# Optimization experiments

Hardware: AMD Instinct MI355X
Metric: run time of the kernel (lower is better)

Reference implementation:

```python
import jax, jax.numpy as jnp
import numpy as np

D_MODEL = 1024
N_HEADS = 16
D_K = D_MODEL // N_HEADS


def setup_inputs() -> dict:
    key = jax.random.key(0)
    ks = jax.random.split(key, 5)
    B, T = 4, 2048
    scale = 1.0 / np.sqrt(D_MODEL)
    return {
        "x": jax.random.normal(ks[0], (B, T, D_MODEL), dtype=jnp.float32),
        "W_q": jax.random.normal(ks[1], (D_MODEL, D_MODEL), dtype=jnp.float32) * scale,
        "W_k": jax.random.normal(ks[2], (D_MODEL, D_MODEL), dtype=jnp.float32) * scale,
        "W_v": jax.random.normal(ks[3], (D_MODEL, D_MODEL), dtype=jnp.float32) * scale,
        "W_o": jax.random.normal(ks[4], (D_MODEL, D_MODEL), dtype=jnp.float32) * scale,
    }


def reference(x, W_q, W_k, W_v, W_o):
    B, T, C = x.shape
    # torch nn.Linear(bias=False): y = x @ W.T
    def proj(W):
        y = jnp.einsum('btc,dc->btd', x, W)
        # (B, T, H, Dk) -> (B, H, T, Dk)
        return y.reshape(B, T, N_HEADS, D_K).transpose(0, 2, 1, 3)

    Q, K, V = proj(W_q), proj(W_k), proj(W_v)
    scores = jnp.einsum('bhqd,bhkd->bhqk', Q, K) / jnp.sqrt(jnp.float32(D_K))
    # causal mask: disallow k > q
    causal = jnp.triu(jnp.ones((T, T), dtype=bool), k=1)
    scores = jnp.where(causal, -jnp.inf, scores)
    attn = jax.nn.softmax(scores, axis=-1)
    out = jnp.einsum('bhqk,bhkd->bhqd', attn, V)  # (B, H, T, Dk)
    out = out.transpose(0, 2, 1, 3).reshape(B, T, C)
    return jnp.einsum('btc,dc->btd', out, W_o)
```

## Files before the change

kernel.cpp:

```cpp
#include <hip/hip_runtime.h>

typedef unsigned short u16;
typedef __attribute__((ext_vector_type(8))) short short8;
typedef __attribute__((ext_vector_type(4))) float f32x4;
typedef __attribute__((ext_vector_type(16))) float f32x16;

__device__ __forceinline__ u16 f2bf(float f) {
    union { float f; unsigned u; } v; v.f = f;
    unsigned r = v.u + 0x7fff + ((v.u >> 16) & 1);
    return (u16)(r >> 16);
}

__device__ __forceinline__ unsigned cvtpk(float lo, float hi) {
    unsigned r;
    asm("v_cvt_pk_bf16_f32 %0, %1, %2" : "=v"(r) : "v"(lo), "v"(hi));
    return r;
}

__device__ __forceinline__ void plswap(unsigned& a, unsigned& b) {
    auto r = __builtin_amdgcn_permlane32_swap((int)a, (int)b, false, false);
    a = (unsigned)r[0]; b = (unsigned)r[1];
}

__device__ __forceinline__ void gload_lds16(const void* g, void* l) {
    __builtin_amdgcn_global_load_lds(
        (const __attribute__((address_space(1))) void*)g,
        (__attribute__((address_space(3))) void*)l, 16, 0, 0);
}

__global__ __launch_bounds__(256) void cvt_all(
    const float* __restrict__ x, const float* __restrict__ wq, const float* __restrict__ wk,
    const float* __restrict__ wv, const float* __restrict__ wo,
    u16* __restrict__ xb, u16* __restrict__ wqb, u16* __restrict__ wkb,
    u16* __restrict__ wvb, u16* __restrict__ wob)
{
    const int b = blockIdx.x;
    const float* src; u16* dst; int base;
    if (b < 8192)       { src = x;  dst = xb;  base = b; }
    else if (b < 9216)  { src = wq; dst = wqb; base = b - 8192; }
    else if (b < 10240) { src = wk; dst = wkb; base = b - 9216; }
    else if (b < 11264) { src = wv; dst = wvb; base = b - 10240; }
    else                { src = wo; dst = wob; base = b - 11264; }
    const int i = base * 256 + threadIdx.x;
    float4 v = ((const float4*)src)[i];
    ushort4 o;
    o.x = f2bf(v.x); o.y = f2bf(v.y); o.z = f2bf(v.z); o.w = f2bf(v.w);
    ((ushort4*)dst)[i] = o;
}

__global__ __launch_bounds__(256) void gemm_qkv(
    const u16* __restrict__ Agl, const u16* __restrict__ Wq, const u16* __restrict__ Wk,
    const u16* __restrict__ Wv, u16* __restrict__ Qo, u16* __restrict__ Ko, u16* __restrict__ Vo)
{
    __shared__ alignas(16) u16 As[128 * 64];
    __shared__ alignas(16) u16 Bs[128 * 64];
    const int tid = threadIdx.x;
    const int lane = tid & 63;
    const int w = tid >> 6;
    const int wr = w >> 1, wc = w & 1;
    const int m0 = blockIdx.y * 128;
    const int n0 = blockIdx.x * 128;
    const int z = blockIdx.z;
    const u16* Bgl = (z == 0) ? Wq : (z == 1) ? Wk : Wv;

    f32x4 acc[4][4] = {};

    for (int kt = 0; kt < 16; ++kt) {
        const int kb = kt * 64;
#pragma unroll
        for (int p = 0; p < 4; ++p) {
            const int row = p * 32 + (tid >> 3);
            const int ke = kb + (((tid & 7) * 8) ^ ((row & 7) * 8));
            gload_lds16(Agl + (size_t)(m0 + row) * 1024 + ke, (char*)As + p * 4096 + w * 1024);
            gload_lds16(Bgl + (size_t)(n0 + row) * 1024 + ke, (char*)Bs + p * 4096 + w * 1024);
        }
        __syncthreads();
#pragma unroll
        for (int ks = 0; ks < 2; ++ks) {
            short8 a[4], b[4];
#pragma unroll
            for (int m = 0; m < 4; ++m) {
                const int row = wr * 64 + m * 16 + (lane & 15);
                const int ke = (ks * 32 + (lane >> 4) * 8) ^ ((row & 7) * 8);
                a[m] = *(const short8*)(&As[row * 64 + ke]);
            }
#pragma unroll
            for (int n = 0; n < 4; ++n) {
                const int row = wc * 64 + n * 16 + (lane & 15);
                const int ke = (ks * 32 + (lane >> 4) * 8) ^ ((row & 7) * 8);
                b[n] = *(const short8*)(&Bs[row * 64 + ke]);
            }
#pragma unroll
            for (int m = 0; m < 4; ++m)
#pragma unroll
                for (int n = 0; n < 4; ++n)
                    acc[m][n] = __builtin_amdgcn_mfma_f32_16x16x32_bf16(a[m], b[n], acc[m][n], 0, 0, 0);
        }
        __syncthreads();
    }
    const float qs = (z == 0) ? 0.18033688011112043f : 1.0f;
#pragma unroll
    for (int m = 0; m < 4; ++m)
#pragma unroll
        for (int n = 0; n < 4; ++n)
#pragma unroll
            for (int r = 0; r < 4; ++r) {
                const int row = m0 + wr * 64 + m * 16 + ((lane >> 4) << 2) + r;
                const int col = n0 + wc * 64 + n * 16 + (lane & 15);
                const u16 bv = f2bf(acc[m][n][r] * qs);
                const int bb = row >> 11, t = row & 2047, h = col >> 6, dk = col & 63;
                if (z == 2) {
                    Vo[((size_t)(bb * 16 + h) * 64 + dk) * 2048 + t] = bv;
                } else {
                    u16* dst = (z == 0) ? Qo : Ko;
                    dst[(((size_t)(bb * 16 + h) * 2048 + t) << 6) + dk] = bv;
                }
            }
}

__global__ __launch_bounds__(256) void gemm_out(
    const u16* __restrict__ Agl, const u16* __restrict__ Bgl, float* __restrict__ Co)
{
    __shared__ alignas(16) u16 As[128 * 64];
    __shared__ alignas(16) u16 Bs[128 * 64];
    const int tid = threadIdx.x;
    const int lane = tid & 63;
    const int w = tid >> 6;
    const int wr = w >> 1, wc = w & 1;
    const int m0 = blockIdx.y * 128;
    const int n0 = blockIdx.x * 128;

    f32x4 acc[4][4] = {};

    for (int kt = 0; kt < 16; ++kt) {
        const int kb = kt * 64;
#pragma unroll
        for (int p = 0; p < 4; ++p) {
            const int row = p * 32 + (tid >> 3);
            const int ke = kb + (((tid & 7) * 8) ^ ((row & 7) * 8));
            gload_lds16(Agl + (size_t)(m0 + row) * 1024 + ke, (char*)As + p * 4096 + w * 1024);
            gload_lds16(Bgl + (size_t)(n0 + row) * 1024 + ke, (char*)Bs + p * 4096 + w * 1024);
        }
        __syncthreads();
#pragma unroll
        for (int ks = 0; ks < 2; ++ks) {
            short8 a[4], b[4];
#pragma unroll
            for (int m = 0; m < 4; ++m) {
                const int row = wr * 64 + m * 16 + (lane & 15);
                const int ke = (ks * 32 + (lane >> 4) * 8) ^ ((row & 7) * 8);
                a[m] = *(const short8*)(&As[row * 64 + ke]);
            }
#pragma unroll
            for (int n = 0; n < 4; ++n) {
                const int row = wc * 64 + n * 16 + (lane & 15);
                const int ke = (ks * 32 + (lane >> 4) * 8) ^ ((row & 7) * 8);
                b[n] = *(const short8*)(&Bs[row * 64 + ke]);
            }
#pragma unroll
            for (int m = 0; m < 4; ++m)
#pragma unroll
                for (int n = 0; n < 4; ++n)
                    acc[m][n] = __builtin_amdgcn_mfma_f32_16x16x32_bf16(a[m], b[n], acc[m][n], 0, 0, 0);
        }
        __syncthreads();
    }
#pragma unroll
    for (int m = 0; m < 4; ++m)
#pragma unroll
        for (int n = 0; n < 4; ++n)
#pragma unroll
            for (int r = 0; r < 4; ++r) {
                const int row = m0 + wr * 64 + m * 16 + ((lane >> 4) << 2) + r;
                const int col = n0 + wc * 64 + n * 16 + (lane & 15);
                Co[(size_t)row * 1024 + col] = acc[m][n][r];
            }
}

__global__ __launch_bounds__(256, 2) void attn_fwd2(
    const u16* __restrict__ Q, const u16* __restrict__ Kg,
    const u16* __restrict__ Vt, u16* __restrict__ O)
{
    __shared__ alignas(16) u16 Ks[2][64 * 64];
    __shared__ alignas(16) u16 Vs[2][64 * 64];
    __shared__ alignas(16) float abuf[4][32];

    const int tid = threadIdx.x;
    const int lane = tid & 63;
    const int w = tid >> 6;
    const int l31 = lane & 31;
    const int hi = lane >> 5;
    const int bid = blockIdx.x;
    const int bh = ((bid & 7) << 3) | ((bid >> 3) & 7);
    const int pairIdx = bid >> 6;
    const size_t hb = (size_t)bh << 17;
    const int bb = bh >> 4, h = bh & 15;

    for (int ci = 0; ci < 2; ++ci) {
        const int qc = ci ? pairIdx : (15 - pairIdx);
        const int q0 = qc * 128;
        const int wq0 = q0 + w * 32;
        const int ntiles = qc * 2 + 2;
        const int qrow = wq0 + l31;

        short8 qf[4];
#pragma unroll
        for (int ks = 0; ks < 4; ++ks)
            qf[ks] = *(const short8*)(&Q[hb + ((size_t)qrow << 6) + ks * 16 + hi * 8]);

        f32x16 o0 = {}, o1 = {};
        float m = -1e30f, lsum = 0.f;

#pragma unroll
        for (int p = 0; p < 2; ++p) {
            const int c = p * 256 + tid;
            const int row = c >> 3;
            const int ke = ((c & 7) * 8) ^ ((row & 7) * 8);
            gload_lds16(&Kg[hb + ((size_t)row << 6) + ke], (char*)Ks[0] + p * 4096 + w * 1024);
            gload_lds16(&Vt[hb + ((size_t)row << 11) + ke], (char*)Vs[0] + p * 4096 + w * 1024);
        }
        __syncthreads();

        for (int t = 0; t < ntiles; ++t) {
            const int cur = t & 1;
            if (t + 1 < ntiles) {
                const int t0n = (t + 1) * 64;
#pragma unroll
                for (int p = 0; p < 2; ++p) {
                    const int c = p * 256 + tid;
                    const int row = c >> 3;
                    const int ke = ((c & 7) * 8) ^ ((row & 7) * 8);
                    gload_lds16(&Kg[hb + ((size_t)(t0n + row) << 6) + ke], (char*)Ks[cur ^ 1] + p * 4096 + w * 1024);
                    gload_lds16(&Vt[hb + ((size_t)row << 11) + t0n + ke], (char*)Vs[cur ^ 1] + p * 4096 + w * 1024);
                }
            }
            const int t0 = t * 64;
            if (t0 <= wq0 + 31) {
                const u16* ks_ = Ks[cur];
                const u16* vs_ = Vs[cur];
                f32x16 s0 = {}, s1 = {};
#pragma unroll
                for (int ks = 0; ks < 4; ++ks) {
                    const int d0 = ks * 16 + hi * 8;
                    const int r0 = l31, r1 = 32 + l31;
                    short8 kf0 = *(const short8*)(&ks_[r0 * 64 + (d0 ^ ((r0 & 7) * 8))]);
                    short8 kf1 = *(const short8*)(&ks_[r1 * 64 + (d0 ^ ((r1 & 7) * 8))]);
                    s0 = __builtin_amdgcn_mfma_f32_32x32x16_bf16(kf0, qf[ks], s0, 0, 0, 0);
                    s1 = __builtin_amdgcn_mfma_f32_32x32x16_bf16(kf1, qf[ks], s1, 0, 0, 0);
                }
                if (t0 + 63 > wq0) {
#pragma unroll
                    for (int r = 0; r < 16; ++r) {
                        const int kva = t0 + (r & 3) + 8 * (r >> 2) + 4 * hi;
                        if (kva > qrow)      s0[r] = -1e30f;
                        if (kva + 32 > qrow) s1[r] = -1e30f;
                    }
                }
                float pm = -1e30f;
#pragma unroll
                for (int r = 0; r < 16; ++r) pm = fmaxf(pm, fmaxf(s0[r], s1[r]));
                pm = fmaxf(pm, __shfl_xor(pm, 32));
                if (__any(pm > m + 8.0f)) {
                    const float mn = fmaxf(m, pm);
                    const float al = exp2f(m - mn);
                    m = mn;
                    lsum *= al;
                    if (hi == 0) abuf[w][l31] = al;
#pragma unroll
                    for (int c = 0; c < 4; ++c) {
                        const f32x4 a4 = *(const f32x4*)(&abuf[w][c * 8 + hi * 4]);
#pragma unroll
                        for (int e = 0; e < 4; ++e) {
                            o0[c * 4 + e] *= a4[e];
                            o1[c * 4 + e] *= a4[e];
                        }
                    }
                }
                float rs = 0.f;
                unsigned pwv[16];
#pragma unroll
                for (int sl = 0; sl < 4; ++sl) {
                    float p[8];
#pragma unroll
                    for (int i = 0; i < 8; ++i) {
                        const float sv = (sl < 2) ? s0[(sl & 1) * 8 + i] : s1[(sl & 1) * 8 + i];
                        p[i] = exp2f(sv - m);
                        rs += p[i];
                    }
                    unsigned w01 = cvtpk(p[0], p[1]);
                    unsigned w23 = cvtpk(p[2], p[3]);
                    unsigned w45 = cvtpk(p[4], p[5]);
                    unsigned w67 = cvtpk(p[6], p[7]);
                    plswap(w01, w45);
                    plswap(w23, w67);
                    pwv[sl * 4 + 0] = w01; pwv[sl * 4 + 1] = w23;
                    pwv[sl * 4 + 2] = w45; pwv[sl * 4 + 3] = w67;
                }
                rs += __shfl_xor(rs, 32);
                lsum += rs;
#pragma unroll
                for (int sl = 0; sl < 4; ++sl) {
                    union { unsigned u[4]; short8 s8; } uu;
                    uu.u[0] = pwv[sl * 4 + 0]; uu.u[1] = pwv[sl * 4 + 1];
                    uu.u[2] = pwv[sl * 4 + 2]; uu.u[3] = pwv[sl * 4 + 3];
                    const int tc = sl * 16 + hi * 8;
                    const int r0 = l31, r1 = 32 + l31;
                    short8 vf0 = *(const short8*)(&vs_[r0 * 64 + (tc ^ ((r0 & 7) * 8))]);
                    short8 vf1 = *(const short8*)(&vs_[r1 * 64 + (tc ^ ((r1 & 7) * 8))]);
                    o0 = __builtin_amdgcn_mfma_f32_32x32x16_bf16(uu.s8, vf0, o0, 0, 0, 0);
                    o1 = __builtin_amdgcn_mfma_f32_32x32x16_bf16(uu.s8, vf1, o1, 0, 0, 0);
                }
            }
            __syncthreads();
        }
        if (hi == 0) abuf[w][l31] = __builtin_amdgcn_rcpf(lsum);
#pragma unroll
        for (int c = 0; c < 4; ++c) {
            const f32x4 a4 = *(const f32x4*)(&abuf[w][c * 8 + hi * 4]);
#pragma unroll
            for (int e = 0; e < 4; ++e) {
                const int r = c * 4 + e;
                const int qr = wq0 + (r & 3) + 8 * (r >> 2) + 4 * hi;
                const size_t rb = ((size_t)(bb * 2048 + qr) << 10) + h * 64;
                O[rb + l31]      = f2bf(o0[r] * a4[e]);
                O[rb + 32 + l31] = f2bf(o1[r] * a4[e]);
            }
        }
    }
}

extern "C" void kernel_launch(void* const* d_in, const int* in_sizes, int n_in,
                              void* d_out, int out_size, void* d_ws, size_t ws_size,
                              hipStream_t stream) {
    const float* x  = (const float*)d_in[0];
    const float* Wq = (const float*)d_in[1];
    const float* Wk = (const float*)d_in[2];
    const float* Wv = (const float*)d_in[3];
    const float* Wo = (const float*)d_in[4];
    char* ws = (char*)d_ws;
    const size_t MB = 1u << 20;
    u16* xb   = (u16*)(ws);
    u16* Ob   = (u16*)(ws);
    u16* wqb  = (u16*)(ws + 16 * MB);
    u16* wkb  = (u16*)(ws + 18 * MB);
    u16* wvb  = (u16*)(ws + 20 * MB);
    u16* wob  = (u16*)(ws + 22 * MB);
    u16* Qws  = (u16*)(ws + 24 * MB);
    u16* Kws  = (u16*)(ws + 40 * MB);
    u16* Vtws = (u16*)(ws + 56 * MB);

    cvt_all<<<12288, 256, 0, stream>>>(x, Wq, Wk, Wv, Wo, xb, wqb, wkb, wvb, wob);
    gemm_qkv<<<dim3(8, 64, 3), 256, 0, stream>>>(xb, wqb, wkb, wvb, Qws, Kws, Vtws);
    attn_fwd2<<<512, 256, 0, stream>>>(Qws, Kws, Vtws, Ob);
    gemm_out<<<dim3(8, 64), 256, 0, stream>>>(Ob, wob, (float*)d_out);
}
```

Baseline: 284.4 us.

## Remap GEMM blocks per XCD, skip masked half-tiles, and raise MFMA priority

Both GEMMs now launch a 1D grid, and block ids are remapped so consecutive blocks on the same XCD share M-rows, which should improve L2 reuse of A and B tiles. In attention, the second 32-key half of a diagonal tile is skipped when it is fully masked, avoiding wasted QK MFMAs, softmax exps and PV MFMAs. s_setprio is raised around the MFMA sections to favour matrix issue across waves. The skip path adds branching, and the partially filled pwv array must still be handled correctly.

```diff
diff --git a/kernel.cpp b/kernel.cpp
--- a/kernel.cpp
+++ b/kernel.cpp
@@ -58,9 +58,15 @@
     const int lane = tid & 63;
     const int w = tid >> 6;
     const int wr = w >> 1, wc = w & 1;
-    const int m0 = blockIdx.y * 128;
-    const int n0 = blockIdx.x * 128;
-    const int z = blockIdx.z;
+    const int bid = blockIdx.x;
+    const int xcd = bid & 7;
+    const int j   = bid >> 3;
+    const int nb  = j & 7;
+    const int rem = j >> 3;
+    const int z   = rem >> 3;
+    const int yb  = (xcd << 3) | (rem & 7);
+    const int m0 = yb * 128;
+    const int n0 = nb * 128;
     const u16* Bgl = (z == 0) ? Wq : (z == 1) ? Wk : Wv;
 
     f32x4 acc[4][4] = {};
@@ -127,8 +133,13 @@
     const int lane = tid & 63;
     const int w = tid >> 6;
     const int wr = w >> 1, wc = w & 1;
-    const int m0 = blockIdx.y * 128;
-    const int n0 = blockIdx.x * 128;
+    const int bid = blockIdx.x;
+    const int xcd = bid & 7;
+    const int j   = bid >> 3;
+    const int nb  = j & 7;
+    const int yb  = (xcd << 3) | (j >> 3);
+    const int m0 = yb * 128;
+    const int n0 = nb * 128;
 
     f32x4 acc[4][4] = {};
 
@@ -238,27 +249,41 @@
             if (t0 <= wq0 + 31) {
                 const u16* ks_ = Ks[cur];
                 const u16* vs_ = Vs[cur];
+                const bool full1 = (t0 + 32 <= wq0 + 31);
                 f32x16 s0 = {}, s1 = {};
+                __builtin_amdgcn_s_setprio(1);
 #pragma unroll
                 for (int ks = 0; ks < 4; ++ks) {
                     const int d0 = ks * 16 + hi * 8;
-                    const int r0 = l31, r1 = 32 + l31;
+                    const int r0 = l31;
                     short8 kf0 = *(const short8*)(&ks_[r0 * 64 + (d0 ^ ((r0 & 7) * 8))]);
-                    short8 kf1 = *(const short8*)(&ks_[r1 * 64 + (d0 ^ ((r1 & 7) * 8))]);
                     s0 = __builtin_amdgcn_mfma_f32_32x32x16_bf16(kf0, qf[ks], s0, 0, 0, 0);
-                    s1 = __builtin_amdgcn_mfma_f32_32x32x16_bf16(kf1, qf[ks], s1, 0, 0, 0);
-                }
+                }
+                if (full1) {
+#pragma unroll
+                    for (int ks = 0; ks < 4; ++ks) {
+                        const int d0 = ks * 16 + hi * 8;
+                        const int r1 = 32 + l31;
+                        short8 kf1 = *(const short8*)(&ks_[r1 * 64 + (d0 ^ ((r1 & 7) * 8))]);
+                        s1 = __builtin_amdgcn_mfma_f32_32x32x16_bf16(kf1, qf[ks], s1, 0, 0, 0);
+                    }
+                }
+                __builtin_amdgcn_s_setprio(0);
                 if (t0 + 63 > wq0) {
 #pragma unroll
                     for (int r = 0; r < 16; ++r) {
                         const int kva = t0 + (r & 3) + 8 * (r >> 2) + 4 * hi;
-                        if (kva > qrow)      s0[r] = -1e30f;
-                        if (kva + 32 > qrow) s1[r] = -1e30f;
+                        if (kva > qrow)                s0[r] = -1e30f;
+                        if (full1 && kva + 32 > qrow)  s1[r] = -1e30f;
                     }
                 }
                 float pm = -1e30f;
 #pragma unroll
-                for (int r = 0; r < 16; ++r) pm = fmaxf(pm, fmaxf(s0[r], s1[r]));
+                for (int r = 0; r < 16; ++r) pm = fmaxf(pm, s0[r]);
+                if (full1) {
+#pragma unroll
+                    for (int r = 0; r < 16; ++r) pm = fmaxf(pm, s1[r]);
+                }
                 pm = fmaxf(pm, __shfl_xor(pm, 32));
                 if (__any(pm > m + 8.0f)) {
                     const float mn = fmaxf(m, pm);
@@ -278,8 +303,10 @@
                 }
                 float rs = 0.f;
                 unsigned pwv[16];
+                const int nsl = full1 ? 4 : 2;
 #pragma unroll
                 for (int sl = 0; sl < 4; ++sl) {
+                    if (sl >= nsl) break;
                     float p[8];
 #pragma unroll
                     for (int i = 0; i < 8; ++i) {
@@ -298,8 +325,10 @@
                 }
                 rs += __shfl_xor(rs, 32);
                 lsum += rs;
+                __builtin_amdgcn_s_setprio(1);
 #pragma unroll
                 for (int sl = 0; sl < 4; ++sl) {
+                    if (sl >= nsl) break;
                     union { unsigned u[4]; short8 s8; } uu;
                     uu.u[0] = pwv[sl * 4 + 0]; uu.u[1] = pwv[sl * 4 + 1];
                     uu.u[2] = pwv[sl * 4 + 2]; uu.u[3] = pwv[sl * 4 + 3];
@@ -310,6 +339,7 @@
                     o0 = __builtin_amdgcn_mfma_f32_32x32x16_bf16(uu.s8, vf0, o0, 0, 0, 0);
                     o1 = __builtin_amdgcn_mfma_f32_32x32x16_bf16(uu.s8, vf1, o1, 0, 0, 0);
                 }
+                __builtin_amdgcn_s_setprio(0);
             }
             __syncthreads();
         }
@@ -350,7 +380,7 @@
     u16* Vtws = (u16*)(ws + 56 * MB);
 
     cvt_all<<<12288, 256, 0, stream>>>(x, Wq, Wk, Wv, Wo, xb, wqb, wkb, wvb, wob);
-    gemm_qkv<<<dim3(8, 64, 3), 256, 0, stream>>>(xb, wqb, wkb, wvb, Qws, Kws, Vtws);
+    gemm_qkv<<<1536, 256, 0, stream>>>(xb, wqb, wkb, wvb, Qws, Kws, Vtws);
     attn_fwd2<<<512, 256, 0, stream>>>(Qws, Kws, Vtws, Ob);
-    gemm_out<<<dim3(8, 64), 256, 0, stream>>>(Ob, wob, (float*)d_out);
-}
+    gemm_out<<<512, 256, 0, stream>>>(Ob, wob, (float*)d_out);
+}
```

After: 270.6 us. 1.05x faster.
